# Kernel tuning notes

Hardware: AMD Instinct MI355X
Metric: run time of the kernel (lower is better)

## Reference

```python
import jax, jax.numpy as jnp
import numpy as np

N = 8192
IN_DIM = 512
OUT_DIM = 512


def setup_inputs() -> dict:
    key = jax.random.key(0)
    kA, kX, k1, k2, k3, k4 = jax.random.split(key, 6)
    A = jax.random.uniform(kA, (N, N), dtype=jnp.float32)  # strictly positive -> nonzero triu
    X = jax.random.normal(kX, (N, IN_DIM), dtype=jnp.float32)
    s = 1.0 / np.sqrt(IN_DIM)
    W1 = jax.random.uniform(k1, (OUT_DIM, IN_DIM), minval=-s, maxval=s, dtype=jnp.float32)  # fc
    b1 = jax.random.uniform(k2, (OUT_DIM,), minval=-s, maxval=s, dtype=jnp.float32)
    W2 = jax.random.uniform(k3, (OUT_DIM, IN_DIM), minval=-s, maxval=s, dtype=jnp.float32)  # fc2
    b2 = jax.random.uniform(k4, (OUT_DIM,), minval=-s, maxval=s, dtype=jnp.float32)
    return {"A": A, "X": X, "W1": W1, "b1": b1, "W2": W2, "b2": b2}


def reference(A, X, W1, b1, W2, b2):
    n = A.shape[0]
    # strictly upper-triangular mask (diagonal=1); with uniform(0,1) fill all these
    # entries are nonzero, so torch.nonzero selects exactly them: m = n(n-1)/2 values.
    triu_mask = jnp.triu(jnp.ones((n, n), dtype=bool), k=1)
    m = n * (n - 1) // 2
    # torch.median = lower median = sorted[(m-1)//2]; pad non-triu entries with +inf
    vals = jnp.where(triu_mask, A, jnp.inf).reshape(-1)
    median_value = jnp.sort(vals)[(m - 1) // 2]
    # A[A < median] = 0
    A_thr = jnp.where(A < median_value, jnp.zeros((), A.dtype), A)
    A_norm = jax.nn.softmax(A_thr, axis=-1)
    fcX = X @ W1.T + b1    # [N, out_dim]
    fc2X = X @ W2.T + b2   # [N, out_dim]
    out = jax.nn.leaky_relu(0.1 * fc2X + 0.9 * (A_norm @ fcX), negative_slope=0.01)
    return out
```

## Files before the change

### kernel.cpp

```cpp
#include <hip/hip_runtime.h>

#define DEVI __device__ __forceinline__

typedef __attribute__((ext_vector_type(8))) short short8;
typedef __attribute__((ext_vector_type(4))) short short4v;
typedef __attribute__((ext_vector_type(4))) float f32x4;

static constexpr int NN = 8192;
static constexpr int DD = 512;
static constexpr unsigned LOB = 0x3EFE0000u;
static constexpr unsigned HIB = 0x3F020000u;
static constexpr long long K_RANK = 16775167LL;

static constexpr size_t WS_HIST = 0;
static constexpr size_t WS_CNT  = 1048576;
static constexpr size_t WS_MED  = 1048832;
static constexpr size_t WS_XB   = 2097152;
static constexpr size_t WS_W1B  = WS_XB  + (size_t)NN * DD * 2;
static constexpr size_t WS_W2B  = WS_W1B + (size_t)DD * DD * 2;
static constexpr size_t WS_FCXT = WS_W2B + (size_t)DD * DD * 2;
static constexpr size_t WS_FC2  = WS_FCXT + (size_t)NN * DD * 2;
static constexpr size_t WS_UP   = WS_FC2 + (size_t)NN * DD * 4;
static constexpr size_t WS_ZP   = WS_UP  + (size_t)4 * NN * DD * 2;

DEVI unsigned short f2bf(float f) {
  unsigned u = __float_as_uint(f);
  u += 0x7fffu + ((u >> 16) & 1u);
  return (unsigned short)(u >> 16);
}
DEVI float bf2f(unsigned short h) { return __uint_as_float(((unsigned)h) << 16); }
DEVI int swz(int row, int kq) { return kq ^ ((row >> 1) & 3); }

DEVI void gl_lds16(const void* g, void* l) {
  __builtin_amdgcn_global_load_lds(
      (const __attribute__((address_space(1))) unsigned*)g,
      (__attribute__((address_space(3))) unsigned*)l, 16, 0, 0);
}

#define VMCNT(n) asm volatile("s_waitcnt vmcnt(" #n ")" ::: "memory")
#define LGKM0 asm volatile("s_waitcnt lgkmcnt(0)" ::: "memory")


DEVI void convert_body(const float* __restrict__ X, const float* __restrict__ W1,
                       const float* __restrict__ W2, unsigned short* __restrict__ Xb,
                       unsigned short* __restrict__ W1b, unsigned short* __restrict__ W2b,
                       int cb, int tid) {
  const long long NX = (long long)NN * DD;
  const long long NW = (long long)DD * DD;
  const long long total4 = (NX + 2 * NW) / 4;
  for (long long q = (long long)cb * 512 + tid; q < total4; q += 65536LL) {
    long long e = q << 2;
    const float4* src; unsigned short* dst; long long off;
    if (e < NX)           { src = (const float4*)X;  dst = Xb;  off = e; }
    else if (e < NX + NW) { src = (const float4*)W1; dst = W1b; off = e - NX; }
    else                  { src = (const float4*)W2; dst = W2b; off = e - NX - NW; }
    float4 v = src[off >> 2];
    ushort4 o;
    o.x = f2bf(v.x); o.y = f2bf(v.y); o.z = f2bf(v.z); o.w = f2bf(v.w);
    *(ushort4*)(dst + off) = o;
  }
}

DEVI void hist_body(const float* __restrict__ A, unsigned* __restrict__ hist,
                    unsigned* __restrict__ below, int hb, int tid) {
  unsigned cnt = 0;
  const float4* A4 = (const float4*)A;
  for (long long q = (long long)hb * 512 + tid; q < 16777216LL; q += 458752LL) {
    long long base = q << 2;
    int row = (int)(base >> 13);
    int col = (int)(base & 8191);
    if (col + 3 <= row) continue;
    float4 v = A4[q];
    float vv[4] = {v.x, v.y, v.z, v.w};
#pragma unroll
    for (int j = 0; j < 4; ++j) {
      if (col + j > row) {
        unsigned u = __float_as_uint(vv[j]);
        if (u < LOB) cnt++;
        else if (u < HIB) atomicAdd(&hist[u - LOB], 1u);
      }
    }
  }
  for (int off = 32; off > 0; off >>= 1) cnt += __shfl_down(cnt, off);
  if ((tid & 63) == 0 && cnt) atomicAdd(below, cnt);
}

__global__ __launch_bounds__(512) void stage1_k(const float* __restrict__ A,
                                                const float* __restrict__ X,
                                                const float* __restrict__ W1,
                                                const float* __restrict__ W2,
                                                unsigned* __restrict__ hist,
                                                unsigned* __restrict__ below,
                                                unsigned short* __restrict__ Xb,
                                                unsigned short* __restrict__ W1b,
                                                unsigned short* __restrict__ W2b) {
  const int bx = blockIdx.x;
  if (bx < 128) convert_body(X, W1, W2, Xb, W1b, W2b, bx, threadIdx.x);
  else          hist_body(A, hist, below, bx - 128, threadIdx.x);
}


template <bool BROW, bool OBF>
DEVI void gemm_small_body(const unsigned short* __restrict__ Am,
                          const unsigned short* __restrict__ Bm,
                          const float* __restrict__ bias, void* __restrict__ outp,
                          int ldout, int m0, int n0, char* apB, char* btB) {
  const int tid = threadIdx.x, lane = tid & 63, w = tid >> 6;
  const int wm = w >> 2, wn = w & 3;
  const int lr = lane & 15, lq = lane >> 4;
  const int rL = lane >> 2, kq = lane & 3;
  f32x4 acc[2][4];
#pragma unroll
  for (int i = 0; i < 2; ++i)
#pragma unroll
    for (int j = 0; j < 4; ++j) acc[i][j] = (f32x4){0.f, 0.f, 0.f, 0.f};

#pragma unroll 1
  for (int kt = 0; kt < 16; ++kt) {
    const int k0 = kt * 32;
    __syncthreads();
    if (w < 4) {
      int r = w * 16 + rL;
      gl_lds16(Am + ((size_t)(m0 + r) * DD + k0 + swz(r, kq) * 8), apB + w * 1024);
    }
#pragma unroll
    for (int i = 0; i < 2; ++i) {
      int blk = w * 2 + i;
      int r = blk * 16 + rL;
      gl_lds16(Bm + ((size_t)(n0 + r) * DD + k0 + swz(r, kq) * 8), btB + blk * 1024);
    }
    __syncthreads();
    short8 a[2], b[4];
#pragma unroll
    for (int fr = 0; fr < 2; ++fr) {
      int r = wm * 32 + fr * 16 + lr;
      a[fr] = *(const short8*)(apB + r * 64 + swz(r, lq) * 16);
    }
#pragma unroll
    for (int fc = 0; fc < 4; ++fc) {
      int r = wn * 64 + fc * 16 + lr;
      b[fc] = *(const short8*)(btB + r * 64 + swz(r, lq) * 16);
    }
#pragma unroll
    for (int fr = 0; fr < 2; ++fr)
#pragma unroll
      for (int fc = 0; fc < 4; ++fc)
        acc[fr][fc] = __builtin_amdgcn_mfma_f32_16x16x32_bf16(a[fr], b[fc], acc[fr][fc], 0, 0, 0);
  }
#pragma unroll
  for (int fr = 0; fr < 2; ++fr)
#pragma unroll
    for (int fc = 0; fc < 4; ++fc)
#pragma unroll
      for (int j = 0; j < 4; ++j) {
        int row = m0 + wm * 32 + fr * 16 + lq * 4 + j;
        int col = n0 + wn * 64 + fc * 16 + lr;
        float v = acc[fr][fc][j] + (BROW ? bias[row] : bias[col]);
        if (OBF) ((unsigned short*)outp)[(size_t)row * ldout + col] = f2bf(v);
        else     ((float*)outp)[(size_t)row * ldout + col] = v;
      }
}

__global__ __launch_bounds__(512, 2) void stage2_k(const unsigned short* __restrict__ Xb,
                                                   const unsigned short* __restrict__ W1b,
                                                   const unsigned short* __restrict__ W2b,
                                                   const float* __restrict__ b1,
                                                   const float* __restrict__ b2,
                                                   unsigned short* __restrict__ fcXT,
                                                   float* __restrict__ fc2) {
  __shared__ alignas(16) char plds[20480];
  const int bx = blockIdx.x;
  if (bx < 256) {
    int m0 = ((bx >> 3) & 7) * 64;
    int n0 = ((bx & 7) | ((bx >> 6) << 3)) * 256;
    gemm_small_body<true, true>(W1b, Xb, b1, (void*)fcXT, NN, m0, n0, plds, plds + 4096);
  } else {
    int q = bx - 256;
    gemm_small_body<false, false>(Xb, W2b, b2, (void*)fc2, DD,
                                  (q >> 1) * 64, (q & 1) * 256, plds, plds + 4096);
  }
}

__global__ __launch_bounds__(1024) void select_k(const unsigned* __restrict__ hist,
                                                 const unsigned* __restrict__ below,
                                                 unsigned* __restrict__ med) {
  __shared__ unsigned ssum[1024];
  __shared__ int owner;
  __shared__ unsigned tg_s;
  const int t = threadIdx.x;
  unsigned own = 0;
  const uint4* h4 = (const uint4*)(hist + t * 256);
#pragma unroll 8
  for (int b = 0; b < 64; ++b) {
    uint4 v = h4[b];
    own += v.x + v.y + v.z + v.w;
  }
  ssum[t] = own;
  __syncthreads();
  for (int off = 1; off < 1024; off <<= 1) {
    unsigned v = (t >= off) ? ssum[t - off] : 0u;
    __syncthreads();
    ssum[t] += v;
    __syncthreads();
  }
  long long target = K_RANK - (long long)(*below);
  unsigned incl = ssum[t];
  unsigned excl = incl - own;
  if (target >= (long long)excl && target < (long long)incl) {
    owner = t;
    tg_s = (unsigned)(target - (long long)excl);
  }
  __syncthreads();
  const int to = owner;
  const unsigned tg = tg_s;
  unsigned v256 = (t < 256) ? hist[to * 256 + t] : 0u;
  __syncthreads();
  if (t < 256) ssum[t] = v256;
  __syncthreads();
  for (int off = 1; off < 256; off <<= 1) {
    unsigned v = (t < 256 && t >= off) ? ssum[t - off] : 0u;
    __syncthreads();
    if (t < 256) ssum[t] += v;
    __syncthreads();
  }
  if (t < 256) {
    unsigned incl2 = ssum[t];
    unsigned excl2 = incl2 - v256;
    if (tg >= excl2 && tg < incl2) *med = LOB + (unsigned)(to * 256 + t);
  }
}

static constexpr int LDS_A0 = 0;
static constexpr int LDS_A1 = 8192;
static constexpr int LDS_B0 = 16384;
static constexpr int LDS_B1 = 49152;

__global__ __launch_bounds__(1024, 4) void main_gemm_k(const float* __restrict__ A,
                                                       const unsigned short* __restrict__ fcXT,
                                                       const unsigned* __restrict__ medp,
                                                       unsigned short* __restrict__ Up,
                                                       float* __restrict__ Zp) {
  __shared__ alignas(16) char lds[81920];
  const int tid = threadIdx.x, lane = tid & 63, w = tid >> 6;
  const int wm = w >> 3, wn = w & 7;
  const int lr = lane & 15, lq = lane >> 4;
  const int fid = blockIdx.x;
  const int xcd = fid & 7;
  const int ks = xcd >> 1;
  const int m0 = (((xcd & 1) << 5) | (fid >> 3)) << 7;
  const int kbase = ks * 2048;
  const float med = __uint_as_float(*medp);
  const int rB = lane >> 2, kqB = lane & 3;
  const int rA = tid >> 3, cqA = tid & 7;
  const float* aRow = A + (size_t)(m0 + rA) * NN;
  const int ldsAw = rA * 64 + swz(rA, cqA >> 1) * 16 + (cqA & 1) * 8;

  float zacc = 0.f;
  f32x4 acc[4][4];
#pragma unroll
  for (int i = 0; i < 4; ++i)
#pragma unroll
    for (int j = 0; j < 4; ++j) acc[i][j] = (f32x4){0.f, 0.f, 0.f, 0.f};
  float4 vA0, vA1;

#define CONV4(V, DST)                                                          \
  {                                                                            \
    float vv[4] = {V.x, V.y, V.z, V.w};                                        \
    short4v pb;                                                                \
    _Pragma("unroll")                                                          \
    for (int j = 0; j < 4; ++j) {                                              \
      float a_ = vv[j];                                                        \
      float p_ = (a_ < med) ? 1.0f : __expf(a_);                               \
      unsigned short h_ = f2bf(p_);                                            \
      pb[j] = (short)h_;                                                       \
      zacc += bf2f(h_);                                                        \
    }                                                                          \
    *(short4v*)(DST) = pb;                                                     \
  }

  {
#pragma unroll
    for (int i = 0; i < 2; ++i) {
      int blk = w * 2 + i;
      int o = blk * 16 + rB;
      gl_lds16(fcXT + ((size_t)o * NN + kbase + swz(o, kqB) * 8), lds + LDS_B0 + blk * 1024);
    }
    float4 t0 = *(const float4*)(aRow + kbase + cqA * 4);
    vA0 = *(const float4*)(aRow + kbase + 32 + cqA * 4);
    CONV4(t0, lds + LDS_A0 + ldsAw);
  }
  __syncthreads();

#define ITER(KT, CUR, NCUR, VAC, VAN)                                          \
  {                                                                            \
    const int kt_ = (KT);                                                      \
    if (kt_ < 63) {                                                            \
      const int k1 = kbase + (kt_ + 1) * 32;                                   \
      _Pragma("unroll")                                                        \
      for (int i = 0; i < 2; ++i) {                                            \
        int blk = w * 2 + i;                                                   \
        int o = blk * 16 + rB;                                                 \
        gl_lds16(fcXT + ((size_t)o * NN + k1 + swz(o, kqB) * 8),               \
                 lds + LDS_B##NCUR + blk * 1024);                              \
      }                                                                        \
      if (kt_ < 62) {                                                          \
        const float* apf = aRow + kbase + (kt_ + 2) * 32 + cqA * 4;            \
        asm volatile("global_load_dwordx4 %0, %1, off"                         \
                     : "=&v"(VAN) : "v"(apf) : "memory");                      \
      }                                                                        \
    }                                                                          \
    short8 af[4], bfr[4];                                                      \
    _Pragma("unroll")                                                          \
    for (int fr = 0; fr < 4; ++fr) {                                           \
      int r = wm * 64 + fr * 16 + lr;                                          \
      af[fr] = *(const short8*)(lds + LDS_A##CUR + r * 64 + swz(r, lq) * 16);  \
    }                                                                          \
    _Pragma("unroll")                                                          \
    for (int fc = 0; fc < 4; ++fc) {                                           \
      int o = wn * 64 + fc * 16 + lr;                                          \
      bfr[fc] = *(const short8*)(lds + LDS_B##CUR + o * 64 + swz(o, lq) * 16); \
    }                                                                          \
    __builtin_amdgcn_s_setprio(1);                                             \
    _Pragma("unroll")                                                          \
    for (int fr = 0; fr < 4; ++fr)                                             \
      _Pragma("unroll")                                                        \
      for (int fc = 0; fc < 4; ++fc)                                           \
        acc[fr][fc] = __builtin_amdgcn_mfma_f32_16x16x32_bf16(af[fr], bfr[fc], \
                                                              acc[fr][fc], 0, 0, 0); \
    __builtin_amdgcn_s_setprio(0);                                             \
    if (kt_ < 63) {                                                            \
      if (kt_ < 62) { VMCNT(3); } else { VMCNT(2); }                           \
      __builtin_amdgcn_sched_barrier(0);                                       \
      CONV4(VAC, lds + LDS_A##NCUR + ldsAw);                                   \
      if (kt_ < 62) { VMCNT(1); } else { VMCNT(0); }                           \
      LGKM0;                                                                   \
      __builtin_amdgcn_s_barrier();                                            \
    }                                                                          \
  }

#pragma unroll 1
  for (int t2 = 0; t2 < 32; ++t2) {
    ITER(2 * t2,     0, 1, vA0, vA1);
    ITER(2 * t2 + 1, 1, 0, vA1, vA0);
  }
#undef ITER
#undef CONV4

  zacc += __shfl_xor(zacc, 1);
  zacc += __shfl_xor(zacc, 2);
  zacc += __shfl_xor(zacc, 4);
  if ((tid & 7) == 0) Zp[(size_t)ks * NN + m0 + rA] = zacc;
#pragma unroll
  for (int fr = 0; fr < 4; ++fr)
#pragma unroll
    for (int fc = 0; fc < 4; ++fc)
#pragma unroll
      for (int j = 0; j < 4; ++j) {
        int row = m0 + wm * 64 + fr * 16 + lq * 4 + j;
        int col = wn * 64 + fc * 16 + lr;
        Up[((size_t)ks << 22) + ((size_t)row << 9) + col] = f2bf(acc[fr][fc][j]);
      }
}

__global__ __launch_bounds__(256) void reduce_k(const unsigned short* __restrict__ Up,
                                                const float* __restrict__ Zp,
                                                const float* __restrict__ fc2,
                                                float* __restrict__ out) {
  long long t = (long long)blockIdx.x * blockDim.x + threadIdx.x;
  if (t >= (long long)NN * DD / 8) return;
  long long base = t << 3;
  int row = (int)(base >> 9);
  float Z = Zp[row] + Zp[NN + row] + Zp[2 * NN + row] + Zp[3 * NN + row];
  float inv = 0.9f / Z;
  float s[8] = {0, 0, 0, 0, 0, 0, 0, 0};
#pragma unroll
  for (int sp = 0; sp < 4; ++sp) {
    const uint4 u = *(const uint4*)(Up + ((long long)sp << 22) + base);
    const unsigned uu[4] = {u.x, u.y, u.z, u.w};
#pragma unroll
    for (int j = 0; j < 4; ++j) {
      s[2 * j]     += __uint_as_float(uu[j] << 16);
      s[2 * j + 1] += __uint_as_float(uu[j] & 0xffff0000u);
    }
  }
  float4 fa = *(const float4*)(fc2 + base);
  float4 fb = *(const float4*)(fc2 + base + 4);
  float fv[8] = {fa.x, fa.y, fa.z, fa.w, fb.x, fb.y, fb.z, fb.w};
  float o[8];
#pragma unroll
  for (int j = 0; j < 8; ++j) {
    float v = 0.1f * fv[j] + inv * s[j];
    o[j] = v >= 0.f ? v : 0.01f * v;
  }
  *(float4*)(out + base)     = (float4){o[0], o[1], o[2], o[3]};
  *(float4*)(out + base + 4) = (float4){o[4], o[5], o[6], o[7]};
}

extern "C" void kernel_launch(void* const* d_in, const int* in_sizes, int n_in,
                              void* d_out, int out_size, void* d_ws, size_t ws_size,
                              hipStream_t stream) {
  const float* A  = (const float*)d_in[0];
  const float* X  = (const float*)d_in[1];
  const float* W1 = (const float*)d_in[2];
  const float* b1 = (const float*)d_in[3];
  const float* W2 = (const float*)d_in[4];
  const float* b2 = (const float*)d_in[5];
  char* ws = (char*)d_ws;
  unsigned* hist = (unsigned*)(ws + WS_HIST);
  unsigned* cnt  = (unsigned*)(ws + WS_CNT);
  unsigned* med  = (unsigned*)(ws + WS_MED);
  unsigned short* Xb   = (unsigned short*)(ws + WS_XB);
  unsigned short* W1b  = (unsigned short*)(ws + WS_W1B);
  unsigned short* W2b  = (unsigned short*)(ws + WS_W2B);
  unsigned short* fcXT = (unsigned short*)(ws + WS_FCXT);
  float* fc2           = (float*)(ws + WS_FC2);
  unsigned short* Upp  = (unsigned short*)(ws + WS_UP);
  float* Zp            = (float*)(ws + WS_ZP);

  hipMemsetAsync(ws, 0, 1048576 + 512, stream);
  hipLaunchKernelGGL(stage1_k, dim3(1024), dim3(512), 0, stream,
                     A, X, W1, W2, hist, cnt, Xb, W1b, W2b);
  hipLaunchKernelGGL(stage2_k, dim3(512), dim3(512), 0, stream,
                     Xb, W1b, W2b, b1, b2, fcXT, fc2);
  hipLaunchKernelGGL(select_k, dim3(1), dim3(1024), 0, stream, hist, cnt, med);
  hipLaunchKernelGGL(main_gemm_k, dim3(256), dim3(1024), 0, stream, A, fcXT, med, Upp, Zp);
  hipLaunchKernelGGL(reduce_k, dim3(2048), dim3(256), 0, stream, Upp, Zp, fc2, (float*)d_out);
}
```

Baseline: 280.0 us.

## Split main GEMM tiles by output-column halves, drop double buffering, use zeroing kernel

Measured after the change: 297.7 us. +6.3%, slower.

```diff
diff --git a/kernel.cpp b/kernel.cpp
--- a/kernel.cpp
+++ b/kernel.cpp
@@ -3,7 +3,6 @@
 #define DEVI __device__ __forceinline__
 
 typedef __attribute__((ext_vector_type(8))) short short8;
-typedef __attribute__((ext_vector_type(4))) short short4v;
 typedef __attribute__((ext_vector_type(4))) float f32x4;
 
 static constexpr int NN = 8192;
@@ -37,8 +36,11 @@
       (__attribute__((address_space(3))) unsigned*)l, 16, 0, 0);
 }
 
-#define VMCNT(n) asm volatile("s_waitcnt vmcnt(" #n ")" ::: "memory")
-#define LGKM0 asm volatile("s_waitcnt lgkmcnt(0)" ::: "memory")
+__global__ __launch_bounds__(256) void zero_k(uint4* __restrict__ hist4,
+                                              unsigned* __restrict__ cntmed) {
+  hist4[blockIdx.x * 256 + threadIdx.x] = (uint4){0u, 0u, 0u, 0u};
+  if (blockIdx.x == 0 && threadIdx.x < 2) cntmed[threadIdx.x * 64] = 0u;
+}
 
 
 DEVI void convert_body(const float* __restrict__ X, const float* __restrict__ W1,
@@ -231,29 +233,31 @@
 }
 
 static constexpr int LDS_A0 = 0;
-static constexpr int LDS_A1 = 8192;
-static constexpr int LDS_B0 = 16384;
-static constexpr int LDS_B1 = 49152;
-
-__global__ __launch_bounds__(1024, 4) void main_gemm_k(const float* __restrict__ A,
-                                                       const unsigned short* __restrict__ fcXT,
-                                                       const unsigned* __restrict__ medp,
-                                                       unsigned short* __restrict__ Up,
-                                                       float* __restrict__ Zp) {
-  __shared__ alignas(16) char lds[81920];
+static constexpr int LDS_B0 = 8192;
+
+__global__ __launch_bounds__(512, 4) void main_gemm_k(const float* __restrict__ A,
+                                                      const unsigned short* __restrict__ fcXT,
+                                                      const unsigned* __restrict__ medp,
+                                                      unsigned short* __restrict__ Up,
+                                                      float* __restrict__ Zp) {
+  __shared__ alignas(16) char lds[24576];
   const int tid = threadIdx.x, lane = tid & 63, w = tid >> 6;
-  const int wm = w >> 3, wn = w & 7;
+  const int wm = w >> 2, wn = w & 3;
   const int lr = lane & 15, lq = lane >> 4;
   const int fid = blockIdx.x;
-  const int xcd = fid & 7;
-  const int ks = xcd >> 1;
-  const int m0 = (((xcd & 1) << 5) | (fid >> 3)) << 7;
+  const int x = fid & 7;
+  const int ks = x >> 1;
+  const int q = fid >> 3;
+  const int nh = q & 1;
+  const int m = (q >> 1) * 2 + (x & 1);
+  const int m0 = m << 7;
+  const int n0 = nh << 8;
   const int kbase = ks * 2048;
   const float med = __uint_as_float(*medp);
   const int rB = lane >> 2, kqB = lane & 3;
-  const int rA = tid >> 3, cqA = tid & 7;
+  const int rA = tid >> 2, cqA = tid & 3;
   const float* aRow = A + (size_t)(m0 + rA) * NN;
-  const int ldsAw = rA * 64 + swz(rA, cqA >> 1) * 16 + (cqA & 1) * 8;
+  const int ldsAw = rA * 64 + swz(rA, cqA) * 16;
 
   float zacc = 0.f;
   f32x4 acc[4][4];
@@ -261,95 +265,59 @@
   for (int i = 0; i < 4; ++i)
 #pragma unroll
     for (int j = 0; j < 4; ++j) acc[i][j] = (f32x4){0.f, 0.f, 0.f, 0.f};
-  float4 vA0, vA1;
-
-#define CONV4(V, DST)                                                          \
-  {                                                                            \
-    float vv[4] = {V.x, V.y, V.z, V.w};                                        \
-    short4v pb;                                                                \
-    _Pragma("unroll")                                                          \
-    for (int j = 0; j < 4; ++j) {                                              \
-      float a_ = vv[j];                                                        \
-      float p_ = (a_ < med) ? 1.0f : __expf(a_);                               \
-      unsigned short h_ = f2bf(p_);                                            \
-      pb[j] = (short)h_;                                                       \
-      zacc += bf2f(h_);                                                        \
-    }                                                                          \
-    *(short4v*)(DST) = pb;                                                     \
-  }
-
-  {
+
+#pragma unroll 1
+  for (int kt = 0; kt < 64; ++kt) {
+    const int k0 = kbase + kt * 32;
+    __syncthreads();
 #pragma unroll
     for (int i = 0; i < 2; ++i) {
       int blk = w * 2 + i;
       int o = blk * 16 + rB;
-      gl_lds16(fcXT + ((size_t)o * NN + kbase + swz(o, kqB) * 8), lds + LDS_B0 + blk * 1024);
-    }
-    float4 t0 = *(const float4*)(aRow + kbase + cqA * 4);
-    vA0 = *(const float4*)(aRow + kbase + 32 + cqA * 4);
-    CONV4(t0, lds + LDS_A0 + ldsAw);
-  }
-  __syncthreads();
-
-#define ITER(KT, CUR, NCUR, VAC, VAN)                                          \
-  {                                                                            \
-    const int kt_ = (KT);                                                      \
-    if (kt_ < 63) {                                                            \
-      const int k1 = kbase + (kt_ + 1) * 32;                                   \
-      _Pragma("unroll")                                                        \
-      for (int i = 0; i < 2; ++i) {                                            \
-        int blk = w * 2 + i;                                                   \
-        int o = blk * 16 + rB;                                                 \
-        gl_lds16(fcXT + ((size_t)o * NN + k1 + swz(o, kqB) * 8),               \
-                 lds + LDS_B##NCUR + blk * 1024);                              \
-      }                                                                        \
-      if (kt_ < 62) {                                                          \
-        const float* apf = aRow + kbase + (kt_ + 2) * 32 + cqA * 4;            \
-        asm volatile("global_load_dwordx4 %0, %1, off"                         \
-                     : "=&v"(VAN) : "v"(apf) : "memory");                      \
-      }                                                                        \
-    }                                                                          \
-    short8 af[4], bfr[4];                                                      \
-    _Pragma("unroll")                                                          \
-    for (int fr = 0; fr < 4; ++fr) {                                           \
-      int r = wm * 64 + fr * 16 + lr;                                          \
-      af[fr] = *(const short8*)(lds + LDS_A##CUR + r * 64 + swz(r, lq) * 16);  \
-    }                                                                          \
-    _Pragma("unroll")                                                          \
-    for (int fc = 0; fc < 4; ++fc) {                                           \
-      int o = wn * 64 + fc * 16 + lr;                                          \
-      bfr[fc] = *(const short8*)(lds + LDS_B##CUR + o * 64 + swz(o, lq) * 16); \
-    }                                                                          \
-    __builtin_amdgcn_s_setprio(1);                                             \
-    _Pragma("unroll")                                                          \
-    for (int fr = 0; fr < 4; ++fr)                                             \
-      _Pragma("unroll")                                                        \
-      for (int fc = 0; fc < 4; ++fc)                                           \
-        acc[fr][fc] = __builtin_amdgcn_mfma_f32_16x16x32_bf16(af[fr], bfr[fc], \
-                                                              acc[fr][fc], 0, 0, 0); \
-    __builtin_amdgcn_s_setprio(0);                                             \
-    if (kt_ < 63) {                                                            \
-      if (kt_ < 62) { VMCNT(3); } else { VMCNT(2); }                           \
-      __builtin_amdgcn_sched_barrier(0);                                       \
-      CONV4(VAC, lds + LDS_A##NCUR + ldsAw);                                   \
-      if (kt_ < 62) { VMCNT(1); } else { VMCNT(0); }                           \
-      LGKM0;                                                                   \
-      __builtin_amdgcn_s_barrier();                                            \
-    }                                                                          \
-  }
-
-#pragma unroll 1
-  for (int t2 = 0; t2 < 32; ++t2) {
-    ITER(2 * t2,     0, 1, vA0, vA1);
-    ITER(2 * t2 + 1, 1, 0, vA1, vA0);
-  }
-#undef ITER
-#undef CONV4
+      gl_lds16(fcXT + ((size_t)(n0 + o) * NN + k0 + swz(o, kqB) * 8),
+               lds + LDS_B0 + blk * 1024);
+    }
+    {
+      const float* ap = aRow + k0 + cqA * 8;
+      float4 v0 = *(const float4*)ap;
+      float4 v1 = *(const float4*)(ap + 4);
+      float vv[8] = {v0.x, v0.y, v0.z, v0.w, v1.x, v1.y, v1.z, v1.w};
+      short8 pb;
+#pragma unroll
+      for (int j = 0; j < 8; ++j) {
+        float a_ = vv[j];
+        float p_ = (a_ < med) ? 1.0f : __expf(a_);
+        unsigned short h_ = f2bf(p_);
+        pb[j] = (short)h_;
+        zacc += bf2f(h_);
+      }
+      *(short8*)(lds + LDS_A0 + ldsAw) = pb;
+    }
+    __syncthreads();
+    short8 af[4], bfr[4];
+#pragma unroll
+    for (int fr = 0; fr < 4; ++fr) {
+      int r = wm * 64 + fr * 16 + lr;
+      af[fr] = *(const short8*)(lds + LDS_A0 + r * 64 + swz(r, lq) * 16);
+    }
+#pragma unroll
+    for (int fc = 0; fc < 4; ++fc) {
+      int o = wn * 64 + fc * 16 + lr;
+      bfr[fc] = *(const short8*)(lds + LDS_B0 + o * 64 + swz(o, lq) * 16);
+    }
+    __builtin_amdgcn_s_setprio(1);
+#pragma unroll
+    for (int fr = 0; fr < 4; ++fr)
+#pragma unroll
+      for (int fc = 0; fc < 4; ++fc)
+        acc[fr][fc] = __builtin_amdgcn_mfma_f32_16x16x32_bf16(af[fr], bfr[fc],
+                                                              acc[fr][fc], 0, 0, 0);
+    __builtin_amdgcn_s_setprio(0);
+  }
 
   zacc += __shfl_xor(zacc, 1);
   zacc += __shfl_xor(zacc, 2);
-  zacc += __shfl_xor(zacc, 4);
-  if ((tid & 7) == 0) Zp[(size_t)ks * NN + m0 + rA] = zacc;
+  if (nh == 0 && (lane & 3) == 0) Zp[(size_t)ks * NN + m0 + rA] = zacc;
 #pragma unroll
   for (int fr = 0; fr < 4; ++fr)
 #pragma unroll
@@ -357,7 +325,7 @@
 #pragma unroll
       for (int j = 0; j < 4; ++j) {
         int row = m0 + wm * 64 + fr * 16 + lq * 4 + j;
-        int col = wn * 64 + fc * 16 + lr;
+        int col = n0 + wn * 64 + fc * 16 + lr;
         Up[((size_t)ks << 22) + ((size_t)row << 9) + col] = f2bf(acc[fr][fc][j]);
       }
 }
@@ -417,12 +385,12 @@
   unsigned short* Upp  = (unsigned short*)(ws + WS_UP);
   float* Zp            = (float*)(ws + WS_ZP);
 
-  hipMemsetAsync(ws, 0, 1048576 + 512, stream);
+  hipLaunchKernelGGL(zero_k, dim3(256), dim3(256), 0, stream, (uint4*)hist, cnt);
   hipLaunchKernelGGL(stage1_k, dim3(1024), dim3(512), 0, stream,
                      A, X, W1, W2, hist, cnt, Xb, W1b, W2b);
   hipLaunchKernelGGL(stage2_k, dim3(512), dim3(512), 0, stream,
                      Xb, W1b, W2b, b1, b2, fcXT, fc2);
   hipLaunchKernelGGL(select_k, dim3(1), dim3(1024), 0, stream, hist, cnt, med);
-  hipLaunchKernelGGL(main_gemm_k, dim3(256), dim3(1024), 0, stream, A, fcXT, med, Upp, Zp);
+  hipLaunchKernelGGL(main_gemm_k, dim3(512), dim3(512), 0, stream, A, fcXT, med, Upp, Zp);
   hipLaunchKernelGGL(reduce_k, dim3(2048), dim3(256), 0, stream, Upp, Zp, fc2, (float*)d_out);
 }
```
